# Performance work log

Measured on AMD Instinct MI355X. Metric: run time of the kernel, lower is better.

The kernel has to match this reference:

```python
import jax, jax.numpy as jnp
import numpy as np

N_HEAD = 16
NEG = -10000.0


def setup_inputs() -> dict:
    key = jax.random.key(0)
    k1, k2, k3 = jax.random.split(key, 3)
    B, S, NX = 2, 2048, 1024
    x = jax.random.normal(k1, (B, S, NX), dtype=jnp.float32)
    # Conv1D weights: y = x @ W + b (HF Conv1D stores weight as [in, out])
    w_attn = jax.random.normal(k2, (NX, 3 * NX), dtype=jnp.float32) * 0.02
    b_attn = jnp.zeros((3 * NX,), dtype=jnp.float32)
    w_proj = jax.random.normal(k3, (NX, NX), dtype=jnp.float32) * 0.02
    b_proj = jnp.zeros((NX,), dtype=jnp.float32)
    return {"x": x, "w_attn": w_attn, "b_attn": b_attn,
            "w_proj": w_proj, "b_proj": b_proj}


def reference(x, w_attn, b_attn, w_proj, b_proj):
    B, S, NX = x.shape
    H = N_HEAD
    D = NX // H  # head dim
    qkv = x @ w_attn + b_attn                      # [B, S, 3*NX]
    q, k, v = jnp.split(qkv, 3, axis=-1)
    # split heads -> [B, H, S, D]
    q = q.reshape(B, S, H, D).transpose(0, 2, 1, 3)
    k = k.reshape(B, S, H, D).transpose(0, 2, 1, 3)
    v = v.reshape(B, S, H, D).transpose(0, 2, 1, 3)
    # scores [B, H, S, S], scaled (scale=True)
    w = jnp.einsum('bhqd,bhkd->bhqk', q, k) / jnp.sqrt(jnp.asarray(D, x.dtype))
    # causal additive mask exactly as the torch code: w*b + NEG*(1-b)
    bias = jnp.tril(jnp.ones((S, S), dtype=x.dtype))[None, None]  # [1,1,S,S]
    w = w * bias + NEG * (1.0 - bias)
    w = jax.nn.softmax(w, axis=-1)
    a = jnp.einsum('bhqk,bhkd->bhqd', w, v)        # [B, H, S, D]
    a = a.transpose(0, 2, 1, 3).reshape(B, S, NX)  # merge heads
    return a @ w_proj + b_proj
```

## Files before the change

### kernel.cpp

```cpp
#include <hip/hip_runtime.h>
#include <cstdint>
#include <cstddef>


typedef __bf16 bf16;
typedef __bf16 bf16x8 __attribute__((ext_vector_type(8)));
typedef __bf16 bf16x4 __attribute__((ext_vector_type(4)));
typedef float f32x4 __attribute__((ext_vector_type(4)));

#define MFMA16(a, b, c) __builtin_amdgcn_mfma_f32_16x16x32_bf16(a, b, c, 0, 0, 0)

typedef const __attribute__((address_space(1))) void* gas_ptr;
typedef __attribute__((address_space(3))) void* las_ptr;
__device__ __forceinline__ void async16(const void* g, void* l) {
    __builtin_amdgcn_global_load_lds((gas_ptr)g, (las_ptr)l, 16, 0, 0);
}
__device__ __forceinline__ float exp2f_fast(float x) { return __builtin_amdgcn_exp2f(x); }

__global__ void cvt_kernel(const float* __restrict__ in, bf16* __restrict__ out, int n) {
    int i = (blockIdx.x * blockDim.x + threadIdx.x) * 4;
    if (i >= n) return;
    float4 v = *reinterpret_cast<const float4*>(in + i);
    bf16x4 o;
    o[0] = (bf16)v.x; o[1] = (bf16)v.y; o[2] = (bf16)v.z; o[3] = (bf16)v.w;
    *reinterpret_cast<bf16x4*>(out + i) = o;
}

__global__ void transpose_kernel(const float* __restrict__ in, bf16* __restrict__ out,
                                 int K, int N) {
    __shared__ float tile[32][33];
    int n0 = blockIdx.x * 32, k0 = blockIdx.y * 32;
    int tx = threadIdx.x, ty = threadIdx.y;
#pragma unroll
    for (int i = 0; i < 32; i += 8)
        tile[ty + i][tx] = in[(size_t)(k0 + ty + i) * N + n0 + tx];
    __syncthreads();
#pragma unroll
    for (int i = 0; i < 32; i += 8)
        out[(size_t)(n0 + ty + i) * K + k0 + tx] = (bf16)tile[tx][ty + i];
}

template <int OUT_BF16>
__global__ __launch_bounds__(256) void gemm_kernel(const bf16* __restrict__ A,
                                                   const bf16* __restrict__ Bt,
                                                   const float* __restrict__ bias,
                                                   void* __restrict__ Cout,
                                                   int M, int N, int K) {
    __shared__ bf16 Alds[2][128 * 32];
    __shared__ bf16 Blds[2][128 * 32];
    const int tid = threadIdx.x;
    const int w = tid >> 6, l = tid & 63;
    const int lane16 = l & 15, quad = l >> 4;
    const int wr = w >> 1, wc = w & 1;
    const int row0 = blockIdx.y * 128, col0 = blockIdx.x * 128;

    const int e = tid * 8;
    const int sr = e >> 5, sc = e & 31;

    f32x4 zero4 = {0.f, 0.f, 0.f, 0.f};
    f32x4 acc[4][4];
#pragma unroll
    for (int i = 0; i < 4; ++i)
#pragma unroll
        for (int j = 0; j < 4; ++j) acc[i][j] = zero4;

#pragma unroll
    for (int ch = 0; ch < 2; ++ch) {
        async16(A + (size_t)(row0 + ch * 64 + sr) * K + sc, &Alds[0][ch * 2048 + e]);
        async16(Bt + (size_t)(col0 + ch * 64 + sr) * K + sc, &Blds[0][ch * 2048 + e]);
    }

    const int niter = K >> 5;
    for (int it = 0; it < niter; ++it) {
        const int cur = it & 1;
        __syncthreads();
        if (it + 1 < niter) {
            const int k1 = (it + 1) << 5;
#pragma unroll
            for (int ch = 0; ch < 2; ++ch) {
                async16(A + (size_t)(row0 + ch * 64 + sr) * K + k1 + sc, &Alds[cur ^ 1][ch * 2048 + e]);
                async16(Bt + (size_t)(col0 + ch * 64 + sr) * K + k1 + sc, &Blds[cur ^ 1][ch * 2048 + e]);
            }
        }
        bf16x8 af[4], bfr[4];
#pragma unroll
        for (int i = 0; i < 4; ++i) {
            af[i] = *reinterpret_cast<const bf16x8*>(&Alds[cur][(64 * wr + 16 * i + lane16) * 32 + quad * 8]);
            bfr[i] = *reinterpret_cast<const bf16x8*>(&Blds[cur][(64 * wc + 16 * i + lane16) * 32 + quad * 8]);
        }
#pragma unroll
        for (int i = 0; i < 4; ++i)
#pragma unroll
            for (int j = 0; j < 4; ++j) acc[i][j] = MFMA16(af[i], bfr[j], acc[i][j]);
    }

#pragma unroll
    for (int i = 0; i < 4; ++i)
#pragma unroll
        for (int j = 0; j < 4; ++j)
#pragma unroll
            for (int r = 0; r < 4; ++r) {
                int row = row0 + 64 * wr + 16 * i + quad * 4 + r;
                int col = col0 + 64 * wc + 16 * j + lane16;
                float v = acc[i][j][r] + bias[col];
                if (OUT_BF16)
                    reinterpret_cast<bf16*>(Cout)[(size_t)row * N + col] = (bf16)v;
                else
                    reinterpret_cast<float*>(Cout)[(size_t)row * N + col] = v;
            }
}

__global__ __launch_bounds__(256) void attn_kernel(const bf16* __restrict__ qkv,
                                                   bf16* __restrict__ aout) {
    const int S = 2048;
    const int bh = blockIdx.x;
    const int b = bh >> 4, h = bh & 15;
    const int p = blockIdx.y;
    const int qH = 31 - p, qL = p;
    const int nkt = qH + 1;
    const int tid = threadIdx.x, w = tid >> 6, l = tid & 63;
    const int lane16 = l & 15, quad = l >> 4;

    __shared__ bf16 Klds[2][64 * 72];
    __shared__ bf16 Vt[2][64 * 72];
    __shared__ bf16 Plds[4][2][16 * 72];

    const bf16* base = qkv + (size_t)b * S * 3072;
    const float qscale = 0.125f * 1.4426950408889634f;
    const float NEGs = -10000.0f * 1.4426950408889634f;

    bf16x8 qfH[2], qfL[2];
#pragma unroll
    for (int hv = 0; hv < 2; ++hv) {
        const bf16* qp = base + (size_t)(qH * 64 + 16 * w + lane16) * 3072 + h * 64;
        bf16x8 t = *reinterpret_cast<const bf16x8*>(qp + hv * 32 + quad * 8);
#pragma unroll
        for (int j = 0; j < 8; ++j) t[j] = (bf16)((float)t[j] * qscale);
        qfH[hv] = t;
        qp = base + (size_t)(qL * 64 + 16 * w + lane16) * 3072 + h * 64;
        t = *reinterpret_cast<const bf16x8*>(qp + hv * 32 + quad * 8);
#pragma unroll
        for (int j = 0; j < 8; ++j) t[j] = (bf16)((float)t[j] * qscale);
        qfL[hv] = t;
    }

    f32x4 zero4 = {0.f, 0.f, 0.f, 0.f};
    f32x4 oH[4], oL[4];
#pragma unroll
    for (int df = 0; df < 4; ++df) { oH[df] = zero4; oL[df] = zero4; }
    float lH = 0.f, lL = 0.f;

    const int kr = tid >> 3, kc = (tid & 7) * 8;
    const int vp = tid & 31, vd = (tid >> 5) * 8;
    bf16x8 kreg0, kreg1, vreg0, vreg1;
    auto load_tile = [&](int kt) {
        const bf16* tb = base + (size_t)(kt * 64) * 3072;
        kreg0 = *reinterpret_cast<const bf16x8*>(tb + (size_t)kr * 3072 + 1024 + h * 64 + kc);
        kreg1 = *reinterpret_cast<const bf16x8*>(tb + (size_t)(32 + kr) * 3072 + 1024 + h * 64 + kc);
        vreg0 = *reinterpret_cast<const bf16x8*>(tb + (size_t)(2 * vp) * 3072 + 2048 + h * 64 + vd);
        vreg1 = *reinterpret_cast<const bf16x8*>(tb + (size_t)(2 * vp + 1) * 3072 + 2048 + h * 64 + vd);
    };

    load_tile(0);
    for (int kt = 0; kt < nkt; ++kt) {
        const int cur = kt & 1;
        *reinterpret_cast<bf16x8*>(&Klds[cur][kr * 72 + kc]) = kreg0;
        *reinterpret_cast<bf16x8*>(&Klds[cur][(32 + kr) * 72 + kc]) = kreg1;
#pragma unroll
        for (int j = 0; j < 8; ++j) {
            union { bf16 h2[2]; uint32_t u; } pk;
            pk.h2[0] = vreg0[j]; pk.h2[1] = vreg1[j];
            *reinterpret_cast<uint32_t*>(&Vt[cur][(vd + j) * 72 + 2 * vp]) = pk.u;
        }
        __syncthreads();
        if (kt + 1 < nkt) load_tile(kt + 1);

        const bool doL = (kt <= qL);

        f32x4 stH[4], stL[4];
#pragma unroll
        for (int kf = 0; kf < 4; ++kf) {
            bf16x8 k0 = *reinterpret_cast<const bf16x8*>(&Klds[cur][(kf * 16 + lane16) * 72 + quad * 8]);
            bf16x8 k1 = *reinterpret_cast<const bf16x8*>(&Klds[cur][(kf * 16 + lane16) * 72 + 32 + quad * 8]);
            f32x4 z = zero4;
            z = MFMA16(k0, qfH[0], z);
            z = MFMA16(k1, qfH[1], z);
            stH[kf] = z;
            if (doL) {
                z = zero4;
                z = MFMA16(k0, qfL[0], z);
                z = MFMA16(k1, qfL[1], z);
                stL[kf] = z;
            }
        }

        {
            if (kt == qH) {
                const int q = qH * 64 + 16 * w + lane16;
#pragma unroll
                for (int kf = 0; kf < 4; ++kf)
#pragma unroll
                    for (int r = 0; r < 4; ++r)
                        if (kt * 64 + kf * 16 + quad * 4 + r > q) stH[kf][r] = NEGs;
            }
            float rs = 0.f;
            bf16* Prow = &Plds[w][0][lane16 * 72];
#pragma unroll
            for (int kf = 0; kf < 4; ++kf) {
                bf16x4 pk;
#pragma unroll
                for (int r = 0; r < 4; ++r) {
                    float pv = exp2f_fast(stH[kf][r]);
                    rs += pv;
                    pk[r] = (bf16)pv;
                }
                *reinterpret_cast<bf16x4*>(Prow + kf * 16 + quad * 4) = pk;
            }
            lH += rs;
        }
        if (doL) {
            if (kt == qL) {
                const int q = qL * 64 + 16 * w + lane16;
#pragma unroll
                for (int kf = 0; kf < 4; ++kf)
#pragma unroll
                    for (int r = 0; r < 4; ++r)
                        if (kt * 64 + kf * 16 + quad * 4 + r > q) stL[kf][r] = NEGs;
            }
            float rs = 0.f;
            bf16* Prow = &Plds[w][1][lane16 * 72];
#pragma unroll
            for (int kf = 0; kf < 4; ++kf) {
                bf16x4 pk;
#pragma unroll
                for (int r = 0; r < 4; ++r) {
                    float pv = exp2f_fast(stL[kf][r]);
                    rs += pv;
                    pk[r] = (bf16)pv;
                }
                *reinterpret_cast<bf16x4*>(Prow + kf * 16 + quad * 4) = pk;
            }
            lL += rs;
        }

#pragma unroll
        for (int kf2 = 0; kf2 < 2; ++kf2) {
            bf16x8 pfH = *reinterpret_cast<const bf16x8*>(
                &Plds[w][0][lane16 * 72 + kf2 * 32 + quad * 8]);
            bf16x8 pfL = *reinterpret_cast<const bf16x8*>(
                &Plds[w][1][lane16 * 72 + kf2 * 32 + quad * 8]);
#pragma unroll
            for (int df = 0; df < 4; ++df) {
                bf16x8 vf = *reinterpret_cast<const bf16x8*>(
                    &Vt[cur][(df * 16 + lane16) * 72 + kf2 * 32 + quad * 8]);
                oH[df] = MFMA16(pfH, vf, oH[df]);
                if (doL) oL[df] = MFMA16(pfL, vf, oL[df]);
            }
        }
    }

    lH += __shfl_xor(lH, 16, 64);
    lH += __shfl_xor(lH, 32, 64);
    lL += __shfl_xor(lL, 16, 64);
    lL += __shfl_xor(lL, 32, 64);
    float invH = 1.0f / lH, invL = 1.0f / lL;

#pragma unroll
    for (int r = 0; r < 4; ++r) {
        float liH = __shfl(invH, quad * 4 + r, 64);
        float liL = __shfl(invL, quad * 4 + r, 64);
        int rowH = qH * 64 + 16 * w + quad * 4 + r;
        int rowL = qL * 64 + 16 * w + quad * 4 + r;
#pragma unroll
        for (int df = 0; df < 4; ++df) {
            aout[(size_t)(b * S + rowH) * 1024 + h * 64 + df * 16 + lane16] =
                (bf16)(oH[df][r] * liH);
            aout[(size_t)(b * S + rowL) * 1024 + h * 64 + df * 16 + lane16] =
                (bf16)(oL[df][r] * liL);
        }
    }
}

extern "C" void kernel_launch(void* const* d_in, const int* in_sizes, int n_in,
                              void* d_out, int out_size, void* d_ws, size_t ws_size,
                              hipStream_t stream) {
    const float* x      = (const float*)d_in[0];
    const float* w_attn = (const float*)d_in[1];
    const float* b_attn = (const float*)d_in[2];
    const float* w_proj = (const float*)d_in[3];
    const float* b_proj = (const float*)d_in[4];
    float* out = (float*)d_out;
    char* ws = (char*)d_ws;

    const int Mtok = 4096, NX = 1024, N3 = 3072;
    bf16* xb   = (bf16*)(ws);
    bf16* wTa  = (bf16*)(ws + ((size_t)8 << 20));
    bf16* wTp  = (bf16*)(ws + ((size_t)14 << 20));
    bf16* qkv  = (bf16*)(ws + ((size_t)16 << 20));
    bf16* abuf = (bf16*)(ws + ((size_t)40 << 20));

    cvt_kernel<<<dim3((Mtok * NX / 4 + 255) / 256), 256, 0, stream>>>(x, xb, Mtok * NX);
    transpose_kernel<<<dim3(N3 / 32, NX / 32), dim3(32, 8), 0, stream>>>(w_attn, wTa, NX, N3);
    transpose_kernel<<<dim3(NX / 32, NX / 32), dim3(32, 8), 0, stream>>>(w_proj, wTp, NX, NX);

    gemm_kernel<1><<<dim3(N3 / 128, Mtok / 128), 256, 0, stream>>>(xb, wTa, b_attn, qkv, Mtok, N3, NX);
    attn_kernel<<<dim3(32, 16), 256, 0, stream>>>(qkv, abuf);
    gemm_kernel<0><<<dim3(NX / 128, Mtok / 128), 256, 0, stream>>>(abuf, wTp, b_proj, out, Mtok, NX, NX);
}
```

Baseline: 188.0 us.

## Split attention into one query tile per block and use 64-row proj GEMM

```diff
diff --git a/kernel.cpp b/kernel.cpp
--- a/kernel.cpp
+++ b/kernel.cpp
@@ -110,45 +110,108 @@
             }
 }
 
+template <int OUT_BF16>
+__global__ __launch_bounds__(256) void gemm64_kernel(const bf16* __restrict__ A,
+                                                     const bf16* __restrict__ Bt,
+                                                     const float* __restrict__ bias,
+                                                     void* __restrict__ Cout,
+                                                     int M, int N, int K) {
+    __shared__ bf16 Alds[2][64 * 32];
+    __shared__ bf16 Blds[2][128 * 32];
+    const int tid = threadIdx.x;
+    const int w = tid >> 6, l = tid & 63;
+    const int lane16 = l & 15, quad = l >> 4;
+    const int wr = w >> 1, wc = w & 1;
+    const int row0 = blockIdx.y * 64, col0 = blockIdx.x * 128;
+
+    const int e = tid * 8;
+    const int sr = e >> 5, sc = e & 31;
+
+    f32x4 zero4 = {0.f, 0.f, 0.f, 0.f};
+    f32x4 acc[2][4];
+#pragma unroll
+    for (int i = 0; i < 2; ++i)
+#pragma unroll
+        for (int j = 0; j < 4; ++j) acc[i][j] = zero4;
+
+    async16(A + (size_t)(row0 + sr) * K + sc, &Alds[0][e]);
+#pragma unroll
+    for (int ch = 0; ch < 2; ++ch)
+        async16(Bt + (size_t)(col0 + ch * 64 + sr) * K + sc, &Blds[0][ch * 2048 + e]);
+
+    const int niter = K >> 5;
+    for (int it = 0; it < niter; ++it) {
+        const int cur = it & 1;
+        __syncthreads();
+        if (it + 1 < niter) {
+            const int k1 = (it + 1) << 5;
+            async16(A + (size_t)(row0 + sr) * K + k1 + sc, &Alds[cur ^ 1][e]);
+#pragma unroll
+            for (int ch = 0; ch < 2; ++ch)
+                async16(Bt + (size_t)(col0 + ch * 64 + sr) * K + k1 + sc, &Blds[cur ^ 1][ch * 2048 + e]);
+        }
+        bf16x8 af[2], bfr[4];
+#pragma unroll
+        for (int i = 0; i < 2; ++i)
+            af[i] = *reinterpret_cast<const bf16x8*>(&Alds[cur][(32 * wr + 16 * i + lane16) * 32 + quad * 8]);
+#pragma unroll
+        for (int j = 0; j < 4; ++j)
+            bfr[j] = *reinterpret_cast<const bf16x8*>(&Blds[cur][(64 * wc + 16 * j + lane16) * 32 + quad * 8]);
+#pragma unroll
+        for (int i = 0; i < 2; ++i)
+#pragma unroll
+            for (int j = 0; j < 4; ++j) acc[i][j] = MFMA16(af[i], bfr[j], acc[i][j]);
+    }
+
+#pragma unroll
+    for (int i = 0; i < 2; ++i)
+#pragma unroll
+        for (int j = 0; j < 4; ++j)
+#pragma unroll
+            for (int r = 0; r < 4; ++r) {
+                int row = row0 + 32 * wr + 16 * i + quad * 4 + r;
+                int col = col0 + 64 * wc + 16 * j + lane16;
+                float v = acc[i][j][r] + bias[col];
+                if (OUT_BF16)
+                    reinterpret_cast<bf16*>(Cout)[(size_t)row * N + col] = (bf16)v;
+                else
+                    reinterpret_cast<float*>(Cout)[(size_t)row * N + col] = v;
+            }
+}
+
 __global__ __launch_bounds__(256) void attn_kernel(const bf16* __restrict__ qkv,
                                                    bf16* __restrict__ aout) {
     const int S = 2048;
     const int bh = blockIdx.x;
     const int b = bh >> 4, h = bh & 15;
-    const int p = blockIdx.y;
-    const int qH = 31 - p, qL = p;
-    const int nkt = qH + 1;
+    const int qt = 31 - blockIdx.y;
+    const int nkt = qt + 1;
     const int tid = threadIdx.x, w = tid >> 6, l = tid & 63;
     const int lane16 = l & 15, quad = l >> 4;
 
-    __shared__ bf16 Klds[2][64 * 72];
-    __shared__ bf16 Vt[2][64 * 72];
-    __shared__ bf16 Plds[4][2][16 * 72];
+    __shared__ bf16 Klds[64 * 72];
+    __shared__ bf16 Vt[64 * 72];
+    __shared__ bf16 Plds[4][16 * 72];
 
     const bf16* base = qkv + (size_t)b * S * 3072;
     const float qscale = 0.125f * 1.4426950408889634f;
     const float NEGs = -10000.0f * 1.4426950408889634f;
 
-    bf16x8 qfH[2], qfL[2];
+    bf16x8 qf[2];
 #pragma unroll
     for (int hv = 0; hv < 2; ++hv) {
-        const bf16* qp = base + (size_t)(qH * 64 + 16 * w + lane16) * 3072 + h * 64;
+        const bf16* qp = base + (size_t)(qt * 64 + 16 * w + lane16) * 3072 + h * 64;
         bf16x8 t = *reinterpret_cast<const bf16x8*>(qp + hv * 32 + quad * 8);
 #pragma unroll
         for (int j = 0; j < 8; ++j) t[j] = (bf16)((float)t[j] * qscale);
-        qfH[hv] = t;
-        qp = base + (size_t)(qL * 64 + 16 * w + lane16) * 3072 + h * 64;
-        t = *reinterpret_cast<const bf16x8*>(qp + hv * 32 + quad * 8);
-#pragma unroll
-        for (int j = 0; j < 8; ++j) t[j] = (bf16)((float)t[j] * qscale);
-        qfL[hv] = t;
+        qf[hv] = t;
     }
 
     f32x4 zero4 = {0.f, 0.f, 0.f, 0.f};
-    f32x4 oH[4], oL[4];
-#pragma unroll
-    for (int df = 0; df < 4; ++df) { oH[df] = zero4; oL[df] = zero4; }
-    float lH = 0.f, lL = 0.f;
+    f32x4 o[4];
+#pragma unroll
+    for (int df = 0; df < 4; ++df) o[df] = zero4;
+    float lsum = 0.f;
 
     const int kr = tid >> 3, kc = (tid & 7) * 8;
     const int vp = tid & 31, vd = (tid >> 5) * 8;
@@ -163,121 +226,78 @@
 
     load_tile(0);
     for (int kt = 0; kt < nkt; ++kt) {
-        const int cur = kt & 1;
-        *reinterpret_cast<bf16x8*>(&Klds[cur][kr * 72 + kc]) = kreg0;
-        *reinterpret_cast<bf16x8*>(&Klds[cur][(32 + kr) * 72 + kc]) = kreg1;
+        __syncthreads();
+        *reinterpret_cast<bf16x8*>(&Klds[kr * 72 + kc]) = kreg0;
+        *reinterpret_cast<bf16x8*>(&Klds[(32 + kr) * 72 + kc]) = kreg1;
 #pragma unroll
         for (int j = 0; j < 8; ++j) {
             union { bf16 h2[2]; uint32_t u; } pk;
             pk.h2[0] = vreg0[j]; pk.h2[1] = vreg1[j];
-            *reinterpret_cast<uint32_t*>(&Vt[cur][(vd + j) * 72 + 2 * vp]) = pk.u;
+            *reinterpret_cast<uint32_t*>(&Vt[(vd + j) * 72 + 2 * vp]) = pk.u;
         }
         __syncthreads();
         if (kt + 1 < nkt) load_tile(kt + 1);
 
-        const bool doL = (kt <= qL);
-
-        f32x4 stH[4], stL[4];
+        f32x4 st[4];
 #pragma unroll
         for (int kf = 0; kf < 4; ++kf) {
-            bf16x8 k0 = *reinterpret_cast<const bf16x8*>(&Klds[cur][(kf * 16 + lane16) * 72 + quad * 8]);
-            bf16x8 k1 = *reinterpret_cast<const bf16x8*>(&Klds[cur][(kf * 16 + lane16) * 72 + 32 + quad * 8]);
+            bf16x8 k0 = *reinterpret_cast<const bf16x8*>(&Klds[(kf * 16 + lane16) * 72 + quad * 8]);
+            bf16x8 k1 = *reinterpret_cast<const bf16x8*>(&Klds[(kf * 16 + lane16) * 72 + 32 + quad * 8]);
             f32x4 z = zero4;
-            z = MFMA16(k0, qfH[0], z);
-            z = MFMA16(k1, qfH[1], z);
-            stH[kf] = z;
-            if (doL) {
-                z = zero4;
-                z = MFMA16(k0, qfL[0], z);
-                z = MFMA16(k1, qfL[1], z);
-                stL[kf] = z;
-            }
-        }
-
-        {
-            if (kt == qH) {
-                const int q = qH * 64 + 16 * w + lane16;
-#pragma unroll
-                for (int kf = 0; kf < 4; ++kf)
-#pragma unroll
-                    for (int r = 0; r < 4; ++r)
-                        if (kt * 64 + kf * 16 + quad * 4 + r > q) stH[kf][r] = NEGs;
-            }
-            float rs = 0.f;
-            bf16* Prow = &Plds[w][0][lane16 * 72];
-#pragma unroll
-            for (int kf = 0; kf < 4; ++kf) {
-                bf16x4 pk;
-#pragma unroll
-                for (int r = 0; r < 4; ++r) {
-                    float pv = exp2f_fast(stH[kf][r]);
-                    rs += pv;
-                    pk[r] = (bf16)pv;
-                }
-                *reinterpret_cast<bf16x4*>(Prow + kf * 16 + quad * 4) = pk;
-            }
-            lH += rs;
-        }
-        if (doL) {
-            if (kt == qL) {
-                const int q = qL * 64 + 16 * w + lane16;
-#pragma unroll
-                for (int kf = 0; kf < 4; ++kf)
-#pragma unroll
-                    for (int r = 0; r < 4; ++r)
-                        if (kt * 64 + kf * 16 + quad * 4 + r > q) stL[kf][r] = NEGs;
-            }
-            float rs = 0.f;
-            bf16* Prow = &Plds[w][1][lane16 * 72];
-#pragma unroll
-            for (int kf = 0; kf < 4; ++kf) {
-                bf16x4 pk;
-#pragma unroll
-                for (int r = 0; r < 4; ++r) {
-                    float pv = exp2f_fast(stL[kf][r]);
-                    rs += pv;
-                    pk[r] = (bf16)pv;
-                }
-                *reinterpret_cast<bf16x4*>(Prow + kf * 16 + quad * 4) = pk;
-            }
-            lL += rs;
-        }
+            z = MFMA16(k0, qf[0], z);
+            z = MFMA16(k1, qf[1], z);
+            st[kf] = z;
+        }
+
+        if (kt == qt) {
+            const int q = qt * 64 + 16 * w + lane16;
+#pragma unroll
+            for (int kf = 0; kf < 4; ++kf)
+#pragma unroll
+                for (int r = 0; r < 4; ++r)
+                    if (kt * 64 + kf * 16 + quad * 4 + r > q) st[kf][r] = NEGs;
+        }
+
+        float rs = 0.f;
+        bf16* Prow = &Plds[w][lane16 * 72];
+#pragma unroll
+        for (int kf = 0; kf < 4; ++kf) {
+            bf16x4 pk;
+#pragma unroll
+            for (int r = 0; r < 4; ++r) {
+                float pv = exp2f_fast(st[kf][r]);
+                rs += pv;
+                pk[r] = (bf16)pv;
+            }
+            *reinterpret_cast<bf16x4*>(Prow + kf * 16 + quad * 4) = pk;
+        }
+        lsum += rs;
 
 #pragma unroll
         for (int kf2 = 0; kf2 < 2; ++kf2) {
-            bf16x8 pfH = *reinterpret_cast<const bf16x8*>(
-                &Plds[w][0][lane16 * 72 + kf2 * 32 + quad * 8]);
-            bf16x8 pfL = *reinterpret_cast<const bf16x8*>(
-                &Plds[w][1][lane16 * 72 + kf2 * 32 + quad * 8]);
+            bf16x8 pf = *reinterpret_cast<const bf16x8*>(
+                &Plds[w][lane16 * 72 + kf2 * 32 + quad * 8]);
 #pragma unroll
             for (int df = 0; df < 4; ++df) {
                 bf16x8 vf = *reinterpret_cast<const bf16x8*>(
-                    &Vt[cur][(df * 16 + lane16) * 72 + kf2 * 32 + quad * 8]);
-                oH[df] = MFMA16(pfH, vf, oH[df]);
-                if (doL) oL[df] = MFMA16(pfL, vf, oL[df]);
-            }
-        }
-    }
-
-    lH += __shfl_xor(lH, 16, 64);
-    lH += __shfl_xor(lH, 32, 64);
-    lL += __shfl_xor(lL, 16, 64);
-    lL += __shfl_xor(lL, 32, 64);
-    float invH = 1.0f / lH, invL = 1.0f / lL;
+                    &Vt[(df * 16 + lane16) * 72 + kf2 * 32 + quad * 8]);
+                o[df] = MFMA16(pf, vf, o[df]);
+            }
+        }
+    }
+
+    lsum += __shfl_xor(lsum, 16, 64);
+    lsum += __shfl_xor(lsum, 32, 64);
+    float inv = 1.0f / lsum;
 
 #pragma unroll
     for (int r = 0; r < 4; ++r) {
-        float liH = __shfl(invH, quad * 4 + r, 64);
-        float liL = __shfl(invL, quad * 4 + r, 64);
-        int rowH = qH * 64 + 16 * w + quad * 4 + r;
-        int rowL = qL * 64 + 16 * w + quad * 4 + r;
-#pragma unroll
-        for (int df = 0; df < 4; ++df) {
-            aout[(size_t)(b * S + rowH) * 1024 + h * 64 + df * 16 + lane16] =
-                (bf16)(oH[df][r] * liH);
-            aout[(size_t)(b * S + rowL) * 1024 + h * 64 + df * 16 + lane16] =
-                (bf16)(oL[df][r] * liL);
-        }
+        float li = __shfl(inv, quad * 4 + r, 64);
+        int row = qt * 64 + 16 * w + quad * 4 + r;
+#pragma unroll
+        for (int df = 0; df < 4; ++df)
+            aout[(size_t)(b * S + row) * 1024 + h * 64 + df * 16 + lane16] =
+                (bf16)(o[df][r] * li);
     }
 }
 
@@ -304,6 +324,6 @@
     transpose_kernel<<<dim3(NX / 32, NX / 32), dim3(32, 8), 0, stream>>>(w_proj, wTp, NX, NX);
 
     gemm_kernel<1><<<dim3(N3 / 128, Mtok / 128), 256, 0, stream>>>(xb, wTa, b_attn, qkv, Mtok, N3, NX);
-    attn_kernel<<<dim3(32, 16), 256, 0, stream>>>(qkv, abuf);
-    gemm_kernel<0><<<dim3(NX / 128, Mtok / 128), 256, 0, stream>>>(abuf, wTp, b_proj, out, Mtok, NX, NX);
-}
+    attn_kernel<<<dim3(32, 32), 256, 0, stream>>>(qkv, abuf);
+    gemm64_kernel<0><<<dim3(NX / 128, Mtok / 64), 256, 0, stream>>>(abuf, wTp, b_proj, out, Mtok, NX, NX);
+}
```

New measurement: 178.3 us. 5.2% less time.
